# Kernel tuning notes

Measured on AMD Instinct MI355X. Metric: run time of the kernel, lower is better.

Reference implementation:

```python
import jax, jax.numpy as jnp
import numpy as np

B, S, N, F = 4, 256, 128, 64
D = 128          # d_model == 2*F so encoder/decoder dims agree
NH = 4           # hard-coded num_heads in both MHA blocks


def _linear(x, w, b):
    # torch nn.Linear: y = x @ W.T + b, W: (out, in)
    return x @ w.T + b


def _mha(q, k, v, w_in, b_in, w_out, b_out, nh):
    # torch nn.MultiheadAttention (batch_first=True) with packed in_proj
    bq, sq, e = q.shape
    hd = e // nh
    qp = _linear(q, w_in[:e], b_in[:e])
    kp = _linear(k, w_in[e:2 * e], b_in[e:2 * e])
    vp = _linear(v, w_in[2 * e:], b_in[2 * e:])
    qh = qp.reshape(bq, sq, nh, hd)
    kh = kp.reshape(bq, k.shape[1], nh, hd)
    vh = vp.reshape(bq, v.shape[1], nh, hd)
    scores = jnp.einsum('bqhd,bkhd->bhqk', qh, kh) / np.sqrt(hd).astype(np.float32)
    attn = jax.nn.softmax(scores, axis=-1)
    out = jnp.einsum('bhqk,bkhd->bqhd', attn, vh).reshape(bq, sq, e)
    return _linear(out, w_out, b_out)


def _pos_enc(s, d):
    pos = jnp.arange(s, dtype=jnp.float32)[:, None]
    div = jnp.exp(jnp.arange(0, d, 2, dtype=jnp.float32) * (-np.log(10000.0) / d))
    pe = jnp.zeros((s, d), dtype=jnp.float32)
    pe = pe.at[:, 0::2].set(jnp.sin(pos * div))
    pe = pe.at[:, 1::2].set(jnp.cos(pos * div))
    return pe


def _haar_decouple(x):
    # exact vectorized pywt haar dwt + single-branch idwt (even seq_len)
    b, s, n, f = x.shape
    pairs = x.reshape(b, s // 2, 2, n, f)
    avg = (pairs[:, :, 0] + pairs[:, :, 1]) * 0.5  # idwt(cA, None) value
    dif = (pairs[:, :, 0] - pairs[:, :, 1]) * 0.5  # idwt(None, cD) value
    x_l = jnp.stack([avg, avg], axis=2).reshape(b, s, n, f)
    x_h = jnp.stack([dif, -dif], axis=2).reshape(b, s, n, f)
    return x_l, x_h


def setup_inputs() -> dict:
    key = jax.random.key(0)
    ks = jax.random.split(key, 32)
    p = lambda i, shp: jax.random.normal(ks[i], shp, jnp.float32) * 0.02
    return {
        'x': jax.random.normal(ks[0], (B, S, N, F), jnp.float32),
        'ts': jax.random.randint(ks[1], (B, S), 0, 252),
        'ta_w_in': p(2, (3 * D, D)), 'ta_b_in': p(3, (3 * D,)),
        'ta_w_out': p(4, (D, D)), 'ta_b_out': p(5, (D,)),
        'conv_w': p(6, (D, 2 * F, 3)), 'conv_b': p(7, (D,)),
        'pl_w': p(8, (D, D)), 'pl_b': p(9, (D,)),
        'ph_w': p(10, (D, D)), 'ph_b': p(11, (D,)),
        'as_w_in': p(12, (3 * D, D)), 'as_b_in': p(13, (3 * D,)),
        'as_w_out': p(14, (D, D)), 'as_b_out': p(15, (D,)),
        'ac_w_in': p(16, (3 * D, D)), 'ac_b_in': p(17, (3 * D,)),
        'ac_w_out': p(18, (D, D)), 'ac_b_out': p(19, (D,)),
        'rl_w': p(20, (1, D)), 'rl_b': p(21, (1,)),
        'cl_w': p(22, (2, D)), 'cl_b': p(23, (2,)),
        'rf_w': p(24, (1, D)), 'rf_b': p(25, (1,)),
        'cf_w': p(26, (2, D)), 'cf_b': p(27, (2,)),
    }


def reference(x, ts, ta_w_in, ta_b_in, ta_w_out, ta_b_out, conv_w, conv_b,
              pl_w, pl_b, ph_w, ph_b, as_w_in, as_b_in, as_w_out, as_b_out,
              ac_w_in, ac_b_in, ac_w_out, ac_b_out, rl_w, rl_b, cl_w, cl_b,
              rf_w, rf_b, cf_w, cf_b):
    b, s, n, f = x.shape
    # --- DecouplingFlowLayer (vectorized haar) ---
    x_l, x_h = _haar_decouple(x)
    xl_cat = jnp.concatenate([x, x_l], axis=-1)  # (b,s,n,2f)
    xh_cat = jnp.concatenate([x, x_h], axis=-1)
    e = 2 * f
    # --- DualFrequencyEncoder ---
    pe = _pos_enc(s, e)
    xl_flat = xl_cat.transpose(0, 2, 1, 3).reshape(b * n, s, e) + pe
    x_tatt = _mha(xl_flat, xl_flat, xl_flat, ta_w_in, ta_b_in, ta_w_out, ta_b_out, NH)
    x_l_gat = x_tatt.reshape(b, s, n, e)  # faithful raw .view() as in torch
    xh_flat = xh_cat.transpose(0, 2, 3, 1).reshape(b * n, e, s)
    conv = jax.lax.conv_general_dilated(
        xh_flat, conv_w, window_strides=(1,), padding=[(2, 2)],
        rhs_dilation=(2,), dimension_numbers=('NCH', 'OIH', 'NCH'))
    conv = jax.nn.relu(conv + conv_b[None, :, None])
    x_h_gat = conv.reshape(b, n, -1, s).transpose(0, 3, 1, 2)  # (b,s,n,D)
    d = x_h_gat.shape[-1]
    # ts -> time_embedding is computed then discarded in the original forward: dead code
    # --- DualFrequencyFusionDecoder ---
    y_l = x_l_gat.reshape(b * n, s, d)
    y_h = x_h_gat.reshape(b * n, s, d)
    q_l = _linear(y_l, pl_w, pl_b)
    k_h = _linear(y_h, ph_w, ph_b)
    y_l2 = _linear(q_l, pl_w, pl_b)  # predictor_l applied twice, as in torch
    lreg = _linear(y_l2, rl_w, rl_b).reshape(b, s, n)
    lcla = jax.nn.softmax(_linear(y_l2, cl_w, cl_b), axis=-1).reshape(b, s, n, 2)
    a_self = _mha(q_l, q_l, q_l, as_w_in, as_b_in, as_w_out, as_b_out, NH)
    a_cross = _mha(q_l, k_h, k_h, ac_w_in, ac_b_in, ac_w_out, ac_b_out, NH)
    fused = (a_self + a_cross).reshape(b, s, n, d)
    reg = _linear(fused, rf_w, rf_b)[..., 0]
    cla = jax.nn.softmax(_linear(fused, cf_w, cf_b), axis=-1)
    return reg, cla, lreg, lcla
```

## Files before the change

### kernel.cpp

```cpp
#include <hip/hip_runtime.h>
#include <hip/hip_bf16.h>

typedef __attribute__((ext_vector_type(8))) short short8v;
typedef __attribute__((ext_vector_type(4))) short short4v;
typedef __attribute__((ext_vector_type(4))) float f32x4;
typedef __hip_bfloat16 bh;

constexpr long SF_ELEMS = 131072L * 128;
#define MFMA16(a, b, c) __builtin_amdgcn_mfma_f32_16x16x32_bf16((a), (b), (c), 0, 0, 0)

__device__ __forceinline__ short bh_bits(float x) {
  bh h = __float2bfloat16(x);
  return *reinterpret_cast<short*>(&h);
}


__global__ __launch_bounds__(256) void sf_wcvt(const float* __restrict__ s0, const float* __restrict__ s1,
                                               const float* __restrict__ s2, const float* __restrict__ s3,
                                               const float* __restrict__ s4, const float* __restrict__ s5,
                                               const float* __restrict__ s6, const float* __restrict__ s7,
                                               const float* __restrict__ cw,
                                               bh* __restrict__ dst, float* __restrict__ pe) {
  int i = blockIdx.x * 256 + threadIdx.x;
  if (i >= 278528) {
    int j = i - 278528;
    if (j < 32768) {
      int e = j & 127, s = j >> 7;
      int ii = e >> 1;
      float dv = expf(-0.0719557945041855f * (float)(2 * ii));
      float ang = (float)s * dv;
      pe[j] = (e & 1) ? cosf(ang) : sinf(ang);
    }
    return;
  }
  float v;
  if      (i <  49152) v = s0[i];
  else if (i <  65536) v = s1[i - 49152];
  else if (i <  81920) v = s2[i - 65536];
  else if (i <  98304) v = s3[i - 81920];
  else if (i < 147456) v = s4[i - 98304];
  else if (i < 163840) v = s5[i - 147456];
  else if (i < 212992) v = s6[i - 163840];
  else if (i < 229376) v = s7[i - 212992];
  else {
    int j = i - 229376;
    int tap = j >> 14, rem = j & 16383;
    v = cw[rem * 3 + tap];
  }
  dst[i] = __float2bfloat16(v);
}

__global__ __launch_bounds__(256) void sf_buildzx(const float* __restrict__ x,
                                                  const float* __restrict__ pe,
                                                  bh* __restrict__ z,
                                                  bh* __restrict__ xh) {
  long i = (long)blockIdx.x * 256 + threadIdx.x;
  if (i >= SF_ELEMS) return;
  int e = (int)(i & 127);
  int s = (int)((i >> 7) & 255);
  int r = (int)(i >> 15);
  int b = r >> 7, stk = r & 127;
  float zv, hv;
  if (e < 64) {
    float val = x[(((long)b * 256 + s) * 128 + stk) * 64 + e];
    zv = val; hv = val;
  } else {
    int f = e - 64;
    int t2 = s >> 1;
    float a0 = x[(((long)b * 256 + 2 * t2) * 128 + stk) * 64 + f];
    float a1 = x[(((long)b * 256 + 2 * t2 + 1) * 128 + stk) * 64 + f];
    zv = 0.5f * (a0 + a1);
    float d = 0.5f * (a0 - a1);
    hv = (s & 1) ? -d : d;
  }
  z[i] = __float2bfloat16(zv + pe[s * 128 + e]);
  xh[i] = __float2bfloat16(hv);
}

__device__ __forceinline__ void attn_body(const bh* Qsrc, const bh* KVsrc,
                                          const bh* __restrict__ Win,
                                          const float* __restrict__ bin,
                                          bh* __restrict__ O, int bn, int h,
                                          bh (*Ks)[36], bh (*Vt)[260],
                                          bh (*Pl)[16][72]) {
  const int t = threadIdx.x, lane = t & 63, w = t >> 6;
  const int lr = lane & 15, lg = lane >> 4;
  const long R0 = (long)bn * 256;
  const int ch = h * 32;
  const f32x4 z4 = {0.f, 0.f, 0.f, 0.f};
  const float SC2 = 0.2550351f;
  short8v aq[4];
  bh* scr = &Pl[w][0][0];
  {
    short8v wq[2][4];
#pragma unroll
    for (int n = 0; n < 2; ++n)
#pragma unroll
      for (int ks = 0; ks < 4; ++ks)
        wq[n][ks] = *reinterpret_cast<const short8v*>(Win + (long)(ch + n * 16 + lr) * 128 + ks * 32 + lg * 8);
#pragma unroll
    for (int m2 = 0; m2 < 4; ++m2) {
      short8v asv[4];
#pragma unroll
      for (int ks = 0; ks < 4; ++ks)
        asv[ks] = *reinterpret_cast<const short8v*>(Qsrc + (R0 + w * 64 + m2 * 16 + lr) * 128 + ks * 32 + lg * 8);
#pragma unroll
      for (int n = 0; n < 2; ++n) {
        f32x4 acc = z4;
#pragma unroll
        for (int ks = 0; ks < 4; ++ks) acc = MFMA16(asv[ks], wq[n][ks], acc);
        float bb = bin[ch + n * 16 + lr];
#pragma unroll
        for (int r = 0; r < 4; ++r)
          scr[(4 * lg + r) * 72 + n * 16 + lr] = __float2bfloat16((acc[r] + bb) * SC2);
      }
      aq[m2] = *reinterpret_cast<const short8v*>(&scr[lr * 72 + lg * 8]);
    }
  }
  {
    short8v wk[2][4], wv[2][4];
#pragma unroll
    for (int n = 0; n < 2; ++n)
#pragma unroll
      for (int ks = 0; ks < 4; ++ks) {
        wk[n][ks] = *reinterpret_cast<const short8v*>(Win + (long)(128 + ch + n * 16 + lr) * 128 + ks * 32 + lg * 8);
        wv[n][ks] = *reinterpret_cast<const short8v*>(Win + (long)(256 + ch + n * 16 + lr) * 128 + ks * 32 + lg * 8);
      }
#pragma unroll
    for (int m2 = 0; m2 < 4; ++m2) {
      short8v asv[4];
#pragma unroll
      for (int ks = 0; ks < 4; ++ks)
        asv[ks] = *reinterpret_cast<const short8v*>(KVsrc + (R0 + w * 64 + m2 * 16 + lr) * 128 + ks * 32 + lg * 8);
#pragma unroll
      for (int n = 0; n < 2; ++n) {
        f32x4 ak = z4, av = z4;
#pragma unroll
        for (int ks = 0; ks < 4; ++ks) {
          ak = MFMA16(asv[ks], wk[n][ks], ak);
          av = MFMA16(asv[ks], wv[n][ks], av);
        }
        float bk = bin[128 + ch + n * 16 + lr];
        float bv = bin[256 + ch + n * 16 + lr];
#pragma unroll
        for (int r = 0; r < 4; ++r)
          Ks[w * 64 + m2 * 16 + 4 * lg + r][n * 16 + lr] = __float2bfloat16(ak[r] + bk);
        short4v pv;
#pragma unroll
        for (int r = 0; r < 4; ++r) pv[r] = bh_bits(av[r] + bv);
        *reinterpret_cast<short4v*>(&Vt[n * 16 + lr][w * 64 + m2 * 16 + 4 * lg]) = pv;
      }
    }
  }
  __syncthreads();
  f32x4 Oacc[4][2];
  float psum[4] = {0.f, 0.f, 0.f, 0.f};
#pragma unroll
  for (int mt = 0; mt < 4; ++mt) { Oacc[mt][0] = z4; Oacc[mt][1] = z4; }
#pragma unroll
  for (int kt = 0; kt < 4; ++kt) {
    short8v bvf[2][2];
#pragma unroll
    for (int dt = 0; dt < 2; ++dt)
#pragma unroll
      for (int ks = 0; ks < 2; ++ks)
        bvf[dt][ks] = *reinterpret_cast<const short8v*>(&Vt[dt * 16 + lr][kt * 64 + ks * 32 + lg * 8]);
#pragma unroll
    for (int mt = 0; mt < 4; ++mt) {
      f32x4 st[4];
#pragma unroll
      for (int nt = 0; nt < 4; ++nt) {
        short8v bk = *reinterpret_cast<const short8v*>(&Ks[kt * 64 + nt * 16 + lr][lg * 8]);
        st[nt] = MFMA16(bk, aq[mt], z4);
      }
      float ps = 0.f;
#pragma unroll
      for (int nt = 0; nt < 4; ++nt) {
        float p0 = exp2f(st[nt][0]);
        float p1 = exp2f(st[nt][1]);
        float p2 = exp2f(st[nt][2]);
        float p3 = exp2f(st[nt][3]);
        ps += (p0 + p1) + (p2 + p3);
        short4v pk;
        pk[0] = bh_bits(p0); pk[1] = bh_bits(p1); pk[2] = bh_bits(p2); pk[3] = bh_bits(p3);
        *reinterpret_cast<short4v*>(&scr[lr * 72 + nt * 16 + 4 * lg]) = pk;
      }
      psum[mt] += ps;
#pragma unroll
      for (int ks = 0; ks < 2; ++ks) {
        short8v ap = *reinterpret_cast<const short8v*>(&scr[lr * 72 + ks * 32 + lg * 8]);
        Oacc[mt][0] = MFMA16(ap, bvf[0][ks], Oacc[mt][0]);
        Oacc[mt][1] = MFMA16(ap, bvf[1][ks], Oacc[mt][1]);
      }
    }
  }
#pragma unroll
  for (int mt = 0; mt < 4; ++mt) {
    float ps = psum[mt];
    ps += __shfl_xor(ps, 16, 64);
    ps += __shfl_xor(ps, 32, 64);
    float inv = 1.f / ps;
#pragma unroll
    for (int r = 0; r < 4; ++r) {
      float invr = __shfl(inv, 4 * lg + r, 64);
      long row = R0 + w * 64 + mt * 16 + 4 * lg + r;
      O[row * 128 + ch + lr]      = __float2bfloat16(Oacc[mt][0][r] * invr);
      O[row * 128 + ch + 16 + lr] = __float2bfloat16(Oacc[mt][1][r] * invr);
    }
  }
}

__device__ __forceinline__ void map_bnh(int g, int& bn, int& h) {
  int xcd = g & 7, slot = g >> 3;
  bn = xcd + 8 * (slot >> 2);
  h = slot & 3;
}

__global__ __launch_bounds__(256) void sf_attnp(const bh* Qsrc, const bh* KVsrc,
                                                const bh* __restrict__ Win,
                                                const float* __restrict__ bin,
                                                bh* __restrict__ O) {
  __shared__ bh Ks[256][36];
  __shared__ bh Vt[32][260];
  __shared__ bh Pl[4][16][72];
  int bn, h;
  map_bnh(blockIdx.x, bn, h);
  attn_body(Qsrc, KVsrc, Win, bin, O, bn, h, Ks, Vt, Pl);
}

__global__ __launch_bounds__(256) void sf_attnp2(const bh* Qc, const bh* KVc,
                                                 const bh* __restrict__ Wc, const float* __restrict__ bc,
                                                 bh* __restrict__ Oc,
                                                 const bh* Qs, const bh* KVs,
                                                 const bh* __restrict__ Wsl, const float* __restrict__ bsl,
                                                 bh* __restrict__ Os) {
  __shared__ bh Ks[256][36];
  __shared__ bh Vt[32][260];
  __shared__ bh Pl[4][16][72];
  int g = blockIdx.x, bn, h;
  if (g < 2048) {
    map_bnh(g, bn, h);
    attn_body(Qc, KVc, Wc, bc, Oc, bn, h, Ks, Vt, Pl);
  } else {
    map_bnh(g - 2048, bn, h);
    attn_body(Qs, KVs, Wsl, bsl, Os, bn, h, Ks, Vt, Pl);
  }
}

__global__ __launch_bounds__(256) void sf_dec(const bh* __restrict__ X,
                                              const bh* __restrict__ Wo, const float* __restrict__ bo,
                                              const bh* __restrict__ Wpl, const float* __restrict__ bpl,
                                              const float* __restrict__ rw, const float* __restrict__ rb,
                                              const float* __restrict__ cw, const float* __restrict__ cb,
                                              bh* __restrict__ Yq, float* __restrict__ out,
                                              long off_reg, long off_cla,
                                              const bh* __restrict__ Xh,
                                              const bh* __restrict__ Wr, const float* __restrict__ cbias,
                                              const bh* __restrict__ Wph, const float* __restrict__ bph,
                                              bh* __restrict__ KH) {
  __shared__ bh Lw[4][32][140];
  __shared__ float hw[3][128];
  const int t = threadIdx.x, lane = t & 63, w = t >> 6;
  const int lr = lane & 15, lg = lane >> 4;
  const f32x4 z4 = {0.f, 0.f, 0.f, 0.f};
  if (blockIdx.x < 1024) {
    const long R0 = (long)blockIdx.x * 128 + w * 32;
    if (t < 128) { hw[0][t] = rw[t]; hw[1][t] = cw[t]; hw[2][t] = cw[128 + t]; }
    {
      short8v a[2][4];
#pragma unroll
      for (int ks = 0; ks < 4; ++ks) {
        a[0][ks] = *reinterpret_cast<const short8v*>(X + (R0 + lr) * 128 + ks * 32 + lg * 8);
        a[1][ks] = *reinterpret_cast<const short8v*>(X + (R0 + 16 + lr) * 128 + ks * 32 + lg * 8);
      }
      f32x4 acc[2][8];
#pragma unroll
      for (int m = 0; m < 2; ++m)
#pragma unroll
        for (int n = 0; n < 8; ++n) acc[m][n] = z4;
#pragma unroll
      for (int ks = 0; ks < 4; ++ks)
#pragma unroll
        for (int n = 0; n < 8; ++n) {
          short8v b = *reinterpret_cast<const short8v*>(Wo + (long)(n * 16 + lr) * 128 + ks * 32 + lg * 8);
          acc[0][n] = MFMA16(a[0][ks], b, acc[0][n]);
          acc[1][n] = MFMA16(a[1][ks], b, acc[1][n]);
        }
#pragma unroll
      for (int n = 0; n < 8; ++n) {
        float bv = bo[n * 16 + lr];
#pragma unroll
        for (int m = 0; m < 2; ++m)
#pragma unroll
          for (int r = 0; r < 4; ++r)
            Lw[w][m * 16 + 4 * lg + r][n * 16 + lr] = __float2bfloat16(acc[m][n][r] + bv);
      }
    }
#pragma unroll
    for (int stage = 0; stage < 2; ++stage) {
      short8v a[2][4];
#pragma unroll
      for (int ks = 0; ks < 4; ++ks) {
        a[0][ks] = *reinterpret_cast<const short8v*>(&Lw[w][lr][ks * 32 + lg * 8]);
        a[1][ks] = *reinterpret_cast<const short8v*>(&Lw[w][16 + lr][ks * 32 + lg * 8]);
      }
      f32x4 acc[2][8];
#pragma unroll
      for (int m = 0; m < 2; ++m)
#pragma unroll
        for (int n = 0; n < 8; ++n) acc[m][n] = z4;
#pragma unroll
      for (int ks = 0; ks < 4; ++ks)
#pragma unroll
        for (int n = 0; n < 8; ++n) {
          short8v b = *reinterpret_cast<const short8v*>(Wpl + (long)(n * 16 + lr) * 128 + ks * 32 + lg * 8);
          acc[0][n] = MFMA16(a[0][ks], b, acc[0][n]);
          acc[1][n] = MFMA16(a[1][ks], b, acc[1][n]);
        }
#pragma unroll
      for (int n = 0; n < 8; ++n) {
        float bv = bpl[n * 16 + lr];
#pragma unroll
        for (int m = 0; m < 2; ++m)
#pragma unroll
          for (int r = 0; r < 4; ++r)
            Lw[w][m * 16 + 4 * lg + r][n * 16 + lr] = __float2bfloat16(acc[m][n][r] + bv);
      }
      if (stage == 0) {
#pragma unroll
        for (int c = 0; c < 8; ++c) {
          int row_l = c * 4 + lg;
          short8v v = *reinterpret_cast<const short8v*>(&Lw[w][row_l][lr * 8]);
          *reinterpret_cast<short8v*>(Yq + (R0 + row_l) * 128 + lr * 8) = v;
        }
      }
    }
    __syncthreads();
    {
      const int rr = lane >> 1, hh = lane & 1;
      float d0 = 0.f, d1 = 0.f, d2 = 0.f;
#pragma unroll
      for (int j = 0; j < 8; ++j) {
        short8v v8 = *reinterpret_cast<const short8v*>(&Lw[w][rr][hh * 64 + j * 8]);
        const bh* vv = reinterpret_cast<const bh*>(&v8);
#pragma unroll
        for (int k = 0; k < 8; ++k) {
          float f = __bfloat162float(vv[k]);
          int c = hh * 64 + j * 8 + k;
          d0 = fmaf(f, hw[0][c], d0);
          d1 = fmaf(f, hw[1][c], d1);
          d2 = fmaf(f, hw[2][c], d2);
        }
      }
      d0 += __shfl_xor(d0, 1, 64);
      d1 += __shfl_xor(d1, 1, 64);
      d2 += __shfl_xor(d2, 1, 64);
      if (hh == 0) {
        long row = R0 + rr;
        d0 += rb[0]; d1 += cb[0]; d2 += cb[1];
        float mx = fmaxf(d1, d2);
        float e1 = __expf(d1 - mx), e2 = __expf(d2 - mx);
        float inv = 1.f / (e1 + e2);
        out[off_reg + row] = d0;
        out[off_cla + row * 2] = e1 * inv;
        out[off_cla + row * 2 + 1] = e2 * inv;
      }
    }
  } else {
    int bid = blockIdx.x - 1024;
    const int bnc = bid >> 1;
    const int half = bid & 1;
    const int b = bnc >> 7, stk = bnc & 127;
    const int R0 = half * 128 + w * 32;
    const short8v zf = {0, 0, 0, 0, 0, 0, 0, 0};
    f32x4 acc[2][8];
#pragma unroll
    for (int m = 0; m < 2; ++m)
#pragma unroll
      for (int n = 0; n < 8; ++n) acc[m][n] = z4;
#pragma unroll
    for (int tap = 0; tap < 3; ++tap) {
      const int shift = 2 * tap - 2;
#pragma unroll
      for (int ks = 0; ks < 4; ++ks) {
        int s0 = R0 + lr + shift;
        int s1 = s0 + 16;
        short8v a0 = zf, a1 = zf;
        if ((unsigned)s0 < 256u)
          a0 = *reinterpret_cast<const short8v*>(Xh + ((long)bnc * 256 + s0) * 128 + ks * 32 + lg * 8);
        if ((unsigned)s1 < 256u)
          a1 = *reinterpret_cast<const short8v*>(Xh + ((long)bnc * 256 + s1) * 128 + ks * 32 + lg * 8);
#pragma unroll
        for (int n = 0; n < 8; ++n) {
          short8v bb = *reinterpret_cast<const short8v*>(Wr + (long)tap * 16384 + (long)(n * 16 + lr) * 128 + ks * 32 + lg * 8);
          acc[0][n] = MFMA16(a0, bb, acc[0][n]);
          acc[1][n] = MFMA16(a1, bb, acc[1][n]);
        }
      }
    }
#pragma unroll
    for (int n = 0; n < 8; ++n) {
      float bv = cbias[n * 16 + lr];
#pragma unroll
      for (int m = 0; m < 2; ++m)
#pragma unroll
        for (int r = 0; r < 4; ++r)
          Lw[w][m * 16 + 4 * lg + r][n * 16 + lr] = __float2bfloat16(fmaxf(acc[m][n][r] + bv, 0.f));
    }
    {
      short8v a2[2][4];
#pragma unroll
      for (int ks = 0; ks < 4; ++ks) {
        a2[0][ks] = *reinterpret_cast<const short8v*>(&Lw[w][lr][ks * 32 + lg * 8]);
        a2[1][ks] = *reinterpret_cast<const short8v*>(&Lw[w][16 + lr][ks * 32 + lg * 8]);
      }
      f32x4 ac2[2][8];
#pragma unroll
      for (int m = 0; m < 2; ++m)
#pragma unroll
        for (int n = 0; n < 8; ++n) ac2[m][n] = z4;
#pragma unroll
      for (int ks = 0; ks < 4; ++ks)
#pragma unroll
        for (int n = 0; n < 8; ++n) {
          short8v b2 = *reinterpret_cast<const short8v*>(Wph + (long)(n * 16 + lr) * 128 + ks * 32 + lg * 8);
          ac2[0][n] = MFMA16(a2[0][ks], b2, ac2[0][n]);
          ac2[1][n] = MFMA16(a2[1][ks], b2, ac2[1][n]);
        }
#pragma unroll
      for (int n = 0; n < 8; ++n) {
        float bv = bph[n * 16 + lr];
#pragma unroll
        for (int m = 0; m < 2; ++m)
#pragma unroll
          for (int r = 0; r < 4; ++r)
            Lw[w][m * 16 + 4 * lg + r][n * 16 + lr] = __float2bfloat16(ac2[m][n][r] + bv);
      }
    }
#pragma unroll
    for (int c = 0; c < 8; ++c) {
      int row_l = c * 4 + lg;
      int sc = R0 + row_l;
      int rp = b * 128 + (sc >> 1);
      int sp = ((sc & 1) << 7) + stk;
      short8v v = *reinterpret_cast<const short8v*>(&Lw[w][row_l][lr * 8]);
      *reinterpret_cast<short8v*>(KH + ((long)rp * 256 + sp) * 128 + lr * 8) = v;
    }
  }
}

__global__ __launch_bounds__(256) void sf_fin2(const bh* __restrict__ Xs,
                                               const bh* __restrict__ Was, const float* __restrict__ bs,
                                               const bh* __restrict__ Xc,
                                               const bh* __restrict__ Wac, const float* __restrict__ bc,
                                               const float* __restrict__ rw, const float* __restrict__ rb,
                                               const float* __restrict__ cw, const float* __restrict__ cb,
                                               float* __restrict__ out, long off_reg, long off_cla) {
  __shared__ bh Lw[4][32][140];
  __shared__ float hw[3][128];
  const int t = threadIdx.x, lane = t & 63, w = t >> 6;
  const int lr = lane & 15, lg = lane >> 4;
  const long R0 = (long)blockIdx.x * 128 + w * 32;
  const f32x4 z4 = {0.f, 0.f, 0.f, 0.f};
  if (t < 128) { hw[0][t] = rw[t]; hw[1][t] = cw[t]; hw[2][t] = cw[128 + t]; }
  {
    f32x4 acc[2][8];
#pragma unroll
    for (int m = 0; m < 2; ++m)
#pragma unroll
      for (int n = 0; n < 8; ++n) acc[m][n] = z4;
    {
      short8v a[2][4];
#pragma unroll
      for (int ks = 0; ks < 4; ++ks) {
        a[0][ks] = *reinterpret_cast<const short8v*>(Xs + (R0 + lr) * 128 + ks * 32 + lg * 8);
        a[1][ks] = *reinterpret_cast<const short8v*>(Xs + (R0 + 16 + lr) * 128 + ks * 32 + lg * 8);
      }
#pragma unroll
      for (int ks = 0; ks < 4; ++ks)
#pragma unroll
        for (int n = 0; n < 8; ++n) {
          short8v b = *reinterpret_cast<const short8v*>(Was + (long)(n * 16 + lr) * 128 + ks * 32 + lg * 8);
          acc[0][n] = MFMA16(a[0][ks], b, acc[0][n]);
          acc[1][n] = MFMA16(a[1][ks], b, acc[1][n]);
        }
    }
    {
      short8v a[2][4];
#pragma unroll
      for (int ks = 0; ks < 4; ++ks) {
        a[0][ks] = *reinterpret_cast<const short8v*>(Xc + (R0 + lr) * 128 + ks * 32 + lg * 8);
        a[1][ks] = *reinterpret_cast<const short8v*>(Xc + (R0 + 16 + lr) * 128 + ks * 32 + lg * 8);
      }
#pragma unroll
      for (int ks = 0; ks < 4; ++ks)
#pragma unroll
        for (int n = 0; n < 8; ++n) {
          short8v b = *reinterpret_cast<const short8v*>(Wac + (long)(n * 16 + lr) * 128 + ks * 32 + lg * 8);
          acc[0][n] = MFMA16(a[0][ks], b, acc[0][n]);
          acc[1][n] = MFMA16(a[1][ks], b, acc[1][n]);
        }
    }
#pragma unroll
    for (int n = 0; n < 8; ++n) {
      float bv = bs[n * 16 + lr] + bc[n * 16 + lr];
#pragma unroll
      for (int m = 0; m < 2; ++m)
#pragma unroll
        for (int r = 0; r < 4; ++r)
          Lw[w][m * 16 + 4 * lg + r][n * 16 + lr] = __float2bfloat16(acc[m][n][r] + bv);
    }
  }
  __syncthreads();
  {
    const int rr = lane >> 1, hh = lane & 1;
    float d0 = 0.f, d1 = 0.f, d2 = 0.f;
#pragma unroll
    for (int j = 0; j < 8; ++j) {
      short8v v8 = *reinterpret_cast<const short8v*>(&Lw[w][rr][hh * 64 + j * 8]);
      const bh* vv = reinterpret_cast<const bh*>(&v8);
#pragma unroll
      for (int k = 0; k < 8; ++k) {
        float f = __bfloat162float(vv[k]);
        int c = hh * 64 + j * 8 + k;
        d0 = fmaf(f, hw[0][c], d0);
        d1 = fmaf(f, hw[1][c], d1);
        d2 = fmaf(f, hw[2][c], d2);
      }
    }
    d0 += __shfl_xor(d0, 1, 64);
    d1 += __shfl_xor(d1, 1, 64);
    d2 += __shfl_xor(d2, 1, 64);
    if (hh == 0) {
      long row = R0 + rr;
      d0 += rb[0]; d1 += cb[0]; d2 += cb[1];
      float mx = fmaxf(d1, d2);
      float e1 = __expf(d1 - mx), e2 = __expf(d2 - mx);
      float inv = 1.f / (e1 + e2);
      out[off_reg + row] = d0;
      out[off_cla + row * 2] = e1 * inv;
      out[off_cla + row * 2 + 1] = e2 * inv;
    }
  }
}

extern "C" void kernel_launch(void* const* d_in, const int* in_sizes, int n_in,
                              void* d_out, int out_size, void* d_ws, size_t ws_size,
                              hipStream_t stream) {
  (void)in_sizes; (void)n_in; (void)out_size; (void)ws_size;
  const float* x       = (const float*)d_in[0];
  const float* ta_w_in = (const float*)d_in[2];
  const float* ta_b_in = (const float*)d_in[3];
  const float* ta_w_o  = (const float*)d_in[4];
  const float* ta_b_o  = (const float*)d_in[5];
  const float* conv_w  = (const float*)d_in[6];
  const float* conv_b  = (const float*)d_in[7];
  const float* pl_w    = (const float*)d_in[8];
  const float* pl_b    = (const float*)d_in[9];
  const float* ph_w    = (const float*)d_in[10];
  const float* ph_b    = (const float*)d_in[11];
  const float* as_w_in = (const float*)d_in[12];
  const float* as_b_in = (const float*)d_in[13];
  const float* as_w_o  = (const float*)d_in[14];
  const float* as_b_o  = (const float*)d_in[15];
  const float* ac_w_in = (const float*)d_in[16];
  const float* ac_b_in = (const float*)d_in[17];
  const float* ac_w_o  = (const float*)d_in[18];
  const float* ac_b_o  = (const float*)d_in[19];
  const float* rl_w    = (const float*)d_in[20];
  const float* rl_b    = (const float*)d_in[21];
  const float* cl_w    = (const float*)d_in[22];
  const float* cl_b    = (const float*)d_in[23];
  const float* rf_w    = (const float*)d_in[24];
  const float* rf_b    = (const float*)d_in[25];
  const float* cf_w    = (const float*)d_in[26];
  const float* cf_b    = (const float*)d_in[27];
  float* out = (float*)d_out;

  bh* S0 = (bh*)d_ws;
  bh* S1 = S0 + SF_ELEMS;
  bh* S2 = S1 + SF_ELEMS;
  bh* S3 = S2 + SF_ELEMS;
  bh* S4 = S3 + SF_ELEMS;
  bh* A  = S4 + SF_ELEMS;
  float* PE = (float*)(A + 278528);

  dim3 blk(256);
  const int GZ = (int)(SF_ELEMS / 256);

  sf_wcvt<<<1216, blk, 0, stream>>>(ta_w_in, ta_w_o, pl_w, ph_w, ac_w_in, ac_w_o,
                                    as_w_in, as_w_o, conv_w, A, PE);
  sf_buildzx<<<GZ, blk, 0, stream>>>(x, PE, S0, S3);
  sf_attnp<<<2048, blk, 0, stream>>>(S0, S0, A, ta_b_in, S1);
  sf_dec<<<2048, blk, 0, stream>>>(S1, A + 49152, ta_b_o, A + 65536, pl_b,
                                   rl_w, rl_b, cl_w, cl_b, S2, out, 393216L, 524288L,
                                   S3, A + 229376, conv_b, A + 81920, ph_b, S4);
  sf_attnp2<<<4096, blk, 0, stream>>>(S2, S4, A + 98304, ac_b_in, S0,
                                      S2, S2, A + 163840, as_b_in, S3);
  sf_fin2<<<1024, blk, 0, stream>>>(S3, A + 212992, as_b_o, S0, A + 147456, ac_b_o,
                                    rf_w, rf_b, cf_w, cf_b, out, 0L, 131072L);
}
```

Baseline: 481.6 us.

## Keep softmax probabilities in registers via ds_bpermute and drop P scratch LDS

The attention kernel no longer writes the exponentiated scores to a per-wave LDS scratch and reads them back. It packs them into bf16 pairs and redistributes them across lanes with ds_bpermute, swapping the PV MFMA operand order so the output comes out transposed. The transposed layout allows vectorized 8-byte output stores without per-row shuffles, and the Q projection scratch reuses the Ks buffer. Dropping the Pl buffer lowers LDS use so launch_bounds can request 4 blocks per CU. The fast exp2 builtin replaces exp2f. The extra permutes and select logic cost instructions, and register pressure under the occupancy hint may cause spills.

```diff
diff --git a/kernel.cpp b/kernel.cpp
--- a/kernel.cpp
+++ b/kernel.cpp
@@ -8,10 +8,15 @@
 
 constexpr long SF_ELEMS = 131072L * 128;
 #define MFMA16(a, b, c) __builtin_amdgcn_mfma_f32_16x16x32_bf16((a), (b), (c), 0, 0, 0)
+#define EXP2F(x) __builtin_amdgcn_exp2f(x)
 
 __device__ __forceinline__ short bh_bits(float x) {
   bh h = __float2bfloat16(x);
   return *reinterpret_cast<short*>(&h);
+}
+__device__ __forceinline__ int pack2bh(float a, float b) {
+  return (int)(((unsigned)(unsigned short)bh_bits(a)) |
+               (((unsigned)(unsigned short)bh_bits(b)) << 16));
 }
 
 
@@ -81,8 +86,7 @@
                                           const bh* __restrict__ Win,
                                           const float* __restrict__ bin,
                                           bh* __restrict__ O, int bn, int h,
-                                          bh (*Ks)[36], bh (*Vt)[260],
-                                          bh (*Pl)[16][72]) {
+                                          bh (*Ks)[36], bh (*Vt)[260]) {
   const int t = threadIdx.x, lane = t & 63, w = t >> 6;
   const int lr = lane & 15, lg = lane >> 4;
   const long R0 = (long)bn * 256;
@@ -90,8 +94,8 @@
   const f32x4 z4 = {0.f, 0.f, 0.f, 0.f};
   const float SC2 = 0.2550351f;
   short8v aq[4];
-  bh* scr = &Pl[w][0][0];
   {
+    bh* scr = &Ks[w * 64][0];
     short8v wq[2][4];
 #pragma unroll
     for (int n = 0; n < 2; ++n)
@@ -112,9 +116,9 @@
         float bb = bin[ch + n * 16 + lr];
 #pragma unroll
         for (int r = 0; r < 4; ++r)
-          scr[(4 * lg + r) * 72 + n * 16 + lr] = __float2bfloat16((acc[r] + bb) * SC2);
-      }
-      aq[m2] = *reinterpret_cast<const short8v*>(&scr[lr * 72 + lg * 8]);
+          scr[(4 * lg + r) * 36 + n * 16 + lr] = __float2bfloat16((acc[r] + bb) * SC2);
+      }
+      aq[m2] = *reinterpret_cast<const short8v*>(&scr[lr * 36 + lg * 8]);
     }
   }
   {
@@ -153,6 +157,9 @@
     }
   }
   __syncthreads();
+  const int addrA = ((2 * (lg & 1)) * 16 + lr) * 4;
+  const int addrB = addrA + 64;
+  const bool hiHalf = (lg >= 2);
   f32x4 Oacc[4][2];
   float psum[4] = {0.f, 0.f, 0.f, 0.f};
 #pragma unroll
@@ -173,24 +180,31 @@
         short8v bk = *reinterpret_cast<const short8v*>(&Ks[kt * 64 + nt * 16 + lr][lg * 8]);
         st[nt] = MFMA16(bk, aq[mt], z4);
       }
+      int pk2[4][2];
       float ps = 0.f;
 #pragma unroll
       for (int nt = 0; nt < 4; ++nt) {
-        float p0 = exp2f(st[nt][0]);
-        float p1 = exp2f(st[nt][1]);
-        float p2 = exp2f(st[nt][2]);
-        float p3 = exp2f(st[nt][3]);
+        float p0 = EXP2F(st[nt][0]);
+        float p1 = EXP2F(st[nt][1]);
+        float p2 = EXP2F(st[nt][2]);
+        float p3 = EXP2F(st[nt][3]);
         ps += (p0 + p1) + (p2 + p3);
-        short4v pk;
-        pk[0] = bh_bits(p0); pk[1] = bh_bits(p1); pk[2] = bh_bits(p2); pk[3] = bh_bits(p3);
-        *reinterpret_cast<short4v*>(&scr[lr * 72 + nt * 16 + 4 * lg]) = pk;
+        pk2[nt][0] = pack2bh(p0, p1);
+        pk2[nt][1] = pack2bh(p2, p3);
       }
       psum[mt] += ps;
 #pragma unroll
       for (int ks = 0; ks < 2; ++ks) {
-        short8v ap = *reinterpret_cast<const short8v*>(&scr[lr * 72 + ks * 32 + lg * 8]);
-        Oacc[mt][0] = MFMA16(ap, bvf[0][ks], Oacc[mt][0]);
-        Oacc[mt][1] = MFMA16(ap, bvf[1][ks], Oacc[mt][1]);
+        union { int i[4]; short8v v; } pf;
+#pragma unroll
+        for (int j = 0; j < 4; ++j) {
+          int ad = (j < 2) ? addrA : addrB;
+          int lo = __builtin_amdgcn_ds_bpermute(ad, pk2[2 * ks][j & 1]);
+          int hi = __builtin_amdgcn_ds_bpermute(ad, pk2[2 * ks + 1][j & 1]);
+          pf.i[j] = hiHalf ? hi : lo;
+        }
+        Oacc[mt][0] = MFMA16(bvf[0][ks], pf.v, Oacc[mt][0]);
+        Oacc[mt][1] = MFMA16(bvf[1][ks], pf.v, Oacc[mt][1]);
       }
     }
   }
@@ -200,12 +214,13 @@
     ps += __shfl_xor(ps, 16, 64);
     ps += __shfl_xor(ps, 32, 64);
     float inv = 1.f / ps;
-#pragma unroll
-    for (int r = 0; r < 4; ++r) {
-      float invr = __shfl(inv, 4 * lg + r, 64);
-      long row = R0 + w * 64 + mt * 16 + 4 * lg + r;
-      O[row * 128 + ch + lr]      = __float2bfloat16(Oacc[mt][0][r] * invr);
-      O[row * 128 + ch + 16 + lr] = __float2bfloat16(Oacc[mt][1][r] * invr);
+    long row = R0 + w * 64 + mt * 16 + lr;
+#pragma unroll
+    for (int dt = 0; dt < 2; ++dt) {
+      short4v ov;
+#pragma unroll
+      for (int r = 0; r < 4; ++r) ov[r] = bh_bits(Oacc[mt][dt][r] * inv);
+      *reinterpret_cast<short4v*>(O + row * 128 + ch + dt * 16 + 4 * lg) = ov;
     }
   }
 }
@@ -216,34 +231,32 @@
   h = slot & 3;
 }
 
-__global__ __launch_bounds__(256) void sf_attnp(const bh* Qsrc, const bh* KVsrc,
-                                                const bh* __restrict__ Win,
-                                                const float* __restrict__ bin,
-                                                bh* __restrict__ O) {
+__global__ __launch_bounds__(256, 4) void sf_attnp(const bh* Qsrc, const bh* KVsrc,
+                                                   const bh* __restrict__ Win,
+                                                   const float* __restrict__ bin,
+                                                   bh* __restrict__ O) {
   __shared__ bh Ks[256][36];
   __shared__ bh Vt[32][260];
-  __shared__ bh Pl[4][16][72];
   int bn, h;
   map_bnh(blockIdx.x, bn, h);
-  attn_body(Qsrc, KVsrc, Win, bin, O, bn, h, Ks, Vt, Pl);
-}
-
-__global__ __launch_bounds__(256) void sf_attnp2(const bh* Qc, const bh* KVc,
-                                                 const bh* __restrict__ Wc, const float* __restrict__ bc,
-                                                 bh* __restrict__ Oc,
-                                                 const bh* Qs, const bh* KVs,
-                                                 const bh* __restrict__ Wsl, const float* __restrict__ bsl,
-                                                 bh* __restrict__ Os) {
+  attn_body(Qsrc, KVsrc, Win, bin, O, bn, h, Ks, Vt);
+}
+
+__global__ __launch_bounds__(256, 4) void sf_attnp2(const bh* Qc, const bh* KVc,
+                                                    const bh* __restrict__ Wc, const float* __restrict__ bc,
+                                                    bh* __restrict__ Oc,
+                                                    const bh* Qs, const bh* KVs,
+                                                    const bh* __restrict__ Wsl, const float* __restrict__ bsl,
+                                                    bh* __restrict__ Os) {
   __shared__ bh Ks[256][36];
   __shared__ bh Vt[32][260];
-  __shared__ bh Pl[4][16][72];
   int g = blockIdx.x, bn, h;
   if (g < 2048) {
     map_bnh(g, bn, h);
-    attn_body(Qc, KVc, Wc, bc, Oc, bn, h, Ks, Vt, Pl);
+    attn_body(Qc, KVc, Wc, bc, Oc, bn, h, Ks, Vt);
   } else {
     map_bnh(g - 2048, bn, h);
-    attn_body(Qs, KVs, Wsl, bsl, Os, bn, h, Ks, Vt, Pl);
+    attn_body(Qs, KVs, Wsl, bsl, Os, bn, h, Ks, Vt);
   }
 }
 
```

Result: slower. 764.3 us (+58.7%).
